# Kernel optimization log

Measured on AMD Instinct MI355X. Metric: run time of the kernel, lower is better.

## Reference

```python
import jax, jax.numpy as jnp
import numpy as np

TOP_K = 1024  # init top_k


def setup_inputs() -> dict:
    key = jax.random.key(0)
    ks = jax.random.split(key, 11)
    B, S, D, H = 8, 1024, 1024, 4096
    s = 0.02
    return {
        "inputs": jax.random.normal(ks[0], (B, S, D), jnp.float32),
        "up_w": jax.random.normal(ks[1], (H, D), jnp.float32) * s,
        "up_b": jax.random.normal(ks[2], (H,), jnp.float32) * s,
        "gate_w1": jax.random.normal(ks[3], (H, D), jnp.float32) * s,
        "gate_b1": jax.random.normal(ks[4], (H,), jnp.float32) * s,
        "gate_w2": jax.random.normal(ks[5], (H, H), jnp.float32) * s,
        "gate_b2": jax.random.normal(ks[6], (H,), jnp.float32) * s,
        "mod_w": jax.random.normal(ks[7], (H, D), jnp.float32) * s,
        "mod_b": jax.random.normal(ks[8], (H,), jnp.float32) * s,
        "down_w": jax.random.normal(ks[9], (D, H), jnp.float32) * s,
        "down_b": jax.random.normal(ks[10], (D,), jnp.float32) * s,
    }


def reference(inputs, up_w, up_b, gate_w1, gate_b1, gate_w2, gate_b2,
              mod_w, mod_b, down_w, down_b):
    B, S, D = inputs.shape
    H = up_w.shape[0]
    # gate: Linear -> ReLU -> Linear, scores [B,S,H]
    scores = jax.nn.relu(jnp.einsum('bsd,hd->bsh', inputs, gate_w1) + gate_b1)
    scores = jnp.einsum('bsh,gh->bsg', scores, gate_w2) + gate_b2
    flat_scores = scores.reshape(B, S * H)
    k = min(TOP_K * S, S * H)
    _, flat_idx = jax.lax.top_k(flat_scores, k)          # [B,k]
    hidden_idx = flat_idx % H                            # [B,k]
    # scatter writes mod.weight[h] at row h -> duplicates harmless -> boolean mask
    batch_idx = jnp.broadcast_to(jnp.arange(B)[:, None], (B, k))
    mask = jnp.zeros((B, H), bool).at[batch_idx, hidden_idx].set(True)
    # per-batch modified weights/bias (materialized like torch repeat+index_put)
    w = jnp.where(mask[:, :, None], mod_w[None], up_w[None])   # [B,H,D]
    b = jnp.where(mask, mod_b[None], up_b[None])               # [B,H]
    h = jnp.einsum('bsd,bhd->bsh', inputs, w) + b[:, None, :]
    h = jax.nn.silu(h)
    # dropout p=0.0 (eval) -> identity
    return jnp.einsum('bsh,dh->bsd', h, down_w) + down_b
```

## Files before the change

kernel.cpp:

```cpp
#include <hip/hip_runtime.h>
#include <cstdint>

typedef __attribute__((ext_vector_type(8))) short short8;
typedef __attribute__((ext_vector_type(4))) float floatx4;
typedef unsigned int uint32;

typedef const void __attribute__((address_space(1)))* gcptr;
typedef void __attribute__((address_space(3)))* lptr;

constexpr int Bn = 8, Sn = 1024, Dn = 1024, Hn = 4096;
constexpr uint32 KTOP = 1024u * 1024u;
constexpr uint32 SKBASE = 0xBB000000u;
constexpr uint32 EMAX = (1u << 27) - 1u;
constexpr uint32 WLO = 3645;
constexpr uint32 WHI = 4157;
constexpr uint32 CAP = 1u << 20;

constexpr size_t NX  = (size_t)Bn * Sn * Dn;
constexpr size_t NW1 = (size_t)Hn * Dn;
constexpr size_t NW2 = (size_t)Hn * Hn;
constexpr size_t NRS = (size_t)Bn * Sn * Hn;

constexpr size_t OFF_XH   = 0;
constexpr size_t OFF_XL   = OFF_XH  + 2 * NX;
constexpr size_t OFF_W1H  = OFF_XL  + 2 * NX;
constexpr size_t OFF_W1L  = OFF_W1H + 2 * NW1;
constexpr size_t OFF_W2H  = OFF_W1L + 2 * NW1;
constexpr size_t OFF_W2L  = OFF_W2H + 2 * NW2;
constexpr size_t OFF_RSH  = OFF_W2L + 2 * NW2;
constexpr size_t OFF_RSL  = OFF_RSH + 2 * NRS;
constexpr size_t OFF_HIST = OFF_RSL + 2 * NRS;
constexpr size_t OFF_HIST2= OFF_HIST + (size_t)Bn * 8192 * 4;
constexpr size_t OFF_HMAX = OFF_HIST2+ (size_t)Bn * 16384 * 4;
constexpr size_t OFF_META = OFF_HMAX + (size_t)Bn * Hn * 4;
constexpr size_t OFF_BSEL = OFF_META + 4096;
constexpr size_t OFF_MASK = OFF_BSEL + (size_t)Bn * Hn * 4;
constexpr size_t WS_SMALL = OFF_MASK + (size_t)Bn * Hn * 4;
constexpr size_t ZERO_BYTES = OFF_BSEL - OFF_HIST;
constexpr size_t OFF_BUF  = OFF_XL;

#define VMCNT(n) asm volatile("s_waitcnt vmcnt(" #n ")" ::: "memory")
#define SCHED0 __builtin_amdgcn_sched_barrier(0)

__device__ __forceinline__ ushort f2bf(float f) {
  uint32 u = __float_as_uint(f);
  u += 0x7fffu + ((u >> 16) & 1u);
  return (ushort)(u >> 16);
}
__device__ __forceinline__ float bf2f(ushort h) {
  return __uint_as_float(((uint32)h) << 16);
}
__device__ __forceinline__ uint32 skey(float v) {
  uint32 u = __float_as_uint(v);
  return (u & 0x80000000u) ? ~u : (u | 0x80000000u);
}
__device__ __forceinline__ uint32 ekey(uint32 key) {
  if (key <= SKBASE) return 0u;
  uint32 d = key - SKBASE;
  return d > EMAX ? EMAX : d;
}
__device__ __forceinline__ void g2l(const ushort* src, ushort* dst) {
  __builtin_amdgcn_global_load_lds((gcptr)src, (lptr)dst, 16, 0, 0);
}
__device__ __forceinline__ void stage_tile(ushort* lds, const ushort* gbase, int ldg, int tid) {
  const int w = tid >> 6;
  const int c0 = tid, c1 = tid + 256;
  g2l(gbase + (size_t)(c0 >> 2) * ldg + (c0 & 3) * 8, lds + (size_t)(w * 64) * 8);
  g2l(gbase + (size_t)(c1 >> 2) * ldg + (c1 & 3) * 8, lds + (size_t)(256 + w * 64) * 8);
}

__global__ __launch_bounds__(256) void cvt_split_k(const float4* __restrict__ x,
                                                   ushort* __restrict__ hi,
                                                   ushort* __restrict__ lo, int n4) {
  int stride = gridDim.x * 256;
  for (int i = blockIdx.x * 256 + threadIdx.x; i < n4; i += stride) {
    float4 v = x[i];
    ushort h0 = f2bf(v.x), h1 = f2bf(v.y), h2 = f2bf(v.z), h3 = f2bf(v.w);
    ushort4 hv; hv.x = h0; hv.y = h1; hv.z = h2; hv.w = h3;
    *(ushort4*)(hi + (size_t)i * 4) = hv;
    ushort4 lv;
    lv.x = f2bf(v.x - bf2f(h0)); lv.y = f2bf(v.y - bf2f(h1));
    lv.z = f2bf(v.z - bf2f(h2)); lv.w = f2bf(v.w - bf2f(h3));
    *(ushort4*)(lo + (size_t)i * 4) = lv;
  }
}
__global__ __launch_bounds__(256) void cvt_single_k(const float4* __restrict__ x,
                                                    ushort* __restrict__ hi, int n4) {
  int stride = gridDim.x * 256;
  for (int i = blockIdx.x * 256 + threadIdx.x; i < n4; i += stride) {
    float4 v = x[i];
    ushort4 hv; hv.x = f2bf(v.x); hv.y = f2bf(v.y); hv.z = f2bf(v.z); hv.w = f2bf(v.w);
    *(ushort4*)(hi + (size_t)i * 4) = hv;
  }
}
__global__ __launch_bounds__(256) void zero_out_k(float* __restrict__ o, int n) {
  int i = blockIdx.x * 256 + threadIdx.x;
  if (i < n) o[i] = 0.f;
}

constexpr int EPI_RELU = 0;
constexpr int EPI_SCORE = 1;
constexpr int EPI_SILU = 2;
constexpr int EPI_F32 = 3;

template <bool SPLIT, bool SELB, int EPI>
__global__ __launch_bounds__(256, SPLIT ? 3 : 2) void gemm_bt(
    const ushort* __restrict__ Ah, const ushort* __restrict__ Al,
    const ushort* __restrict__ Bh, const ushort* __restrict__ Bl,
    const uint32* __restrict__ bmask,
    int N, int K, long long a_bs, long long o_bs, long long bias_bs,
    const float* __restrict__ bias,
    void* __restrict__ outp, void* __restrict__ out2p) {
  __shared__ __align__(16) ushort lds[SPLIT ? 16384 : 8192];
  ushort* As = lds;
  ushort* Bs = lds + (SPLIT ? 8192 : 4096);

  const int tid = threadIdx.x;
  const int w = tid >> 6, l = tid & 63;
  const int wm = (w >> 1) << 6, wn = (w & 1) << 6;
  const int lm = l & 15, lq = l >> 4;
  const int m0 = blockIdx.y << 7, n0 = blockIdx.x << 7;
  const int z = blockIdx.z;

  const ushort* pAh = Ah + (size_t)z * a_bs + (size_t)m0 * K;
  const ushort* pBh = Bh + (size_t)n0 * K;

  floatx4 acc[4][4];
#pragma unroll
  for (int i = 0; i < 4; i++)
#pragma unroll
    for (int j = 0; j < 4; j++) acc[i][j] = floatx4{0.f, 0.f, 0.f, 0.f};

  for (int k0 = 0; k0 < K; k0 += 32) {
    stage_tile(As, pAh + k0, K, tid);
    stage_tile(Bs, pBh + k0, K, tid);
    __syncthreads();
    short8 afh[4], bfh[4];
#pragma unroll
    for (int i = 0; i < 4; i++)
      afh[i] = *(const short8*)&As[(wm + i * 16 + lm) * 32 + lq * 8];
#pragma unroll
    for (int i = 0; i < 4; i++)
      bfh[i] = *(const short8*)&Bs[(wn + i * 16 + lm) * 32 + lq * 8];
#pragma unroll
    for (int mi = 0; mi < 4; mi++)
#pragma unroll
      for (int ni = 0; ni < 4; ni++)
        acc[mi][ni] = __builtin_amdgcn_mfma_f32_16x16x32_bf16(afh[mi], bfh[ni], acc[mi][ni], 0, 0, 0);
    __syncthreads();
  }

  if constexpr (EPI == EPI_SILU) {
    ushort* o = (ushort*)outp + (size_t)z * o_bs;
    const float* bb = bias + (size_t)z * bias_bs;
#pragma unroll
    for (int mi = 0; mi < 4; mi++)
#pragma unroll
      for (int ni = 0; ni < 4; ni++) {
        int gm = m0 + wm + mi * 16 + lq * 4;
        int gn = n0 + wn + ni * 16 + lm;
        float bnv = bb[gn];
#pragma unroll
        for (int r = 0; r < 4; r++) {
          float v = acc[mi][ni][r] + bnv;
          float s = v / (1.f + __expf(-v));
          o[(size_t)(gm + r) * N + gn] = f2bf(s);
        }
      }
  } else if constexpr (EPI == EPI_F32) {
    float* o = (float*)outp;
#pragma unroll
    for (int mi = 0; mi < 4; mi++)
#pragma unroll
      for (int ni = 0; ni < 4; ni++) {
        int gm = m0 + wm + mi * 16 + lq * 4;
        int gn = n0 + wn + ni * 16 + lm;
        float bnv = bias[gn];
#pragma unroll
        for (int r = 0; r < 4; r++)
          o[(size_t)(gm + r) * N + gn] = acc[mi][ni][r] + bnv;
      }
  }
}

__device__ __forceinline__ short8 fragld(const ushort* S, int r, int swz) {
  return *(const short8*)&S[r * 32 + swz];
}
__device__ __forceinline__ void mfma_block(floatx4 (&acc)[8][4], const short8 (&af)[4],
                                           int mi0, const short8 (&bf)[4]) {
#pragma unroll
  for (int mi = 0; mi < 4; mi++)
#pragma unroll
    for (int ni = 0; ni < 4; ni++)
      acc[mi0 + mi][ni] =
          __builtin_amdgcn_mfma_f32_16x16x32_bf16(af[mi], bf[ni], acc[mi0 + mi][ni], 0, 0, 0);
}

template <bool ST>
__device__ __forceinline__ void kstep3(
    floatx4 (&acc)[8][4], ushort* ldsb, int p, int ko,
    const ushort* sAh0, const ushort* sAh1, const ushort* sBh0, const ushort* sBh1,
    const ushort* sAl0, const ushort* sAl1, const ushort* sBl0, const ushort* sBl1,
    int dbase, int swz, int lm, int wrow, int wcol,
    short8 (&ahT)[4], short8 (&bh)[4]) {
  const int q = p ^ 1;
  const ushort* AhS = ldsb + (p * 4 + 0) * 8192;
  const ushort* AlS = ldsb + (p * 4 + 2) * 8192;
  const ushort* BlS = ldsb + (p * 4 + 3) * 8192;
  ushort* dAh = ldsb + (q * 4 + 0) * 8192;
  ushort* dBh = ldsb + (q * 4 + 1) * 8192;
  ushort* dAl = ldsb + (q * 4 + 2) * 8192;
  ushort* dBl = ldsb + (q * 4 + 3) * 8192;

  short8 ahB[4], bl[4];
  __builtin_amdgcn_s_barrier();
  SCHED0;
#pragma unroll
  for (int i = 0; i < 4; i++) ahB[i] = fragld(AhS, wrow + 64 + i * 16 + lm, swz);
#pragma unroll
  for (int i = 0; i < 4; i++) bl[i] = fragld(BlS, wcol + i * 16 + lm, swz);
  if constexpr (ST) {
    g2l(sAh0 + ko, dAh + dbase); g2l(sAh1 + ko, dAh + dbase + 4096);
    g2l(sBh0 + ko, dBh + dbase); g2l(sBh1 + ko, dBh + dbase + 4096);
    g2l(sBl0 + ko, dBl + dbase); g2l(sBl1 + ko, dBl + dbase + 4096);
  }
  SCHED0;
  __builtin_amdgcn_s_setprio(1);
  mfma_block(acc, ahT, 0, bh);
  mfma_block(acc, ahB, 4, bh);
  __builtin_amdgcn_s_setprio(0);
  if constexpr (ST) VMCNT(6); else VMCNT(0);

  short8 alT[4], alB[4];
  __builtin_amdgcn_s_barrier();
  SCHED0;
#pragma unroll
  for (int i = 0; i < 4; i++) alT[i] = fragld(AlS, wrow + i * 16 + lm, swz);
#pragma unroll
  for (int i = 0; i < 4; i++) alB[i] = fragld(AlS, wrow + 64 + i * 16 + lm, swz);
  if constexpr (ST) {
    g2l(sAl0 + ko, dAl + dbase); g2l(sAl1 + ko, dAl + dbase + 4096);
  }
  SCHED0;
  __builtin_amdgcn_s_setprio(1);
  mfma_block(acc, ahT, 0, bl);
  mfma_block(acc, ahB, 4, bl);
  __builtin_amdgcn_s_setprio(0);
  if constexpr (ST) VMCNT(4);

  __builtin_amdgcn_s_barrier();
  SCHED0;
  short8 ahTn[4], bhn[4];
  if constexpr (ST) {
    const ushort* AhSn = ldsb + (q * 4 + 0) * 8192;
    const ushort* BhSn = ldsb + (q * 4 + 1) * 8192;
#pragma unroll
    for (int i = 0; i < 4; i++) ahTn[i] = fragld(AhSn, wrow + i * 16 + lm, swz);
#pragma unroll
    for (int i = 0; i < 4; i++) bhn[i] = fragld(BhSn, wcol + i * 16 + lm, swz);
  }
  SCHED0;
  __builtin_amdgcn_s_setprio(1);
  mfma_block(acc, alT, 0, bh);
  mfma_block(acc, alB, 4, bh);
  __builtin_amdgcn_s_setprio(0);
  if constexpr (ST) {
    VMCNT(2);
#pragma unroll
    for (int i = 0; i < 4; i++) { ahT[i] = ahTn[i]; bh[i] = bhn[i]; }
  }
}

template <bool ST>
__device__ __forceinline__ void kstep_ns(
    floatx4 (&acc)[8][4], ushort* ldsb, int p, int ko,
    const ushort* sA0, const ushort* sA1, const ushort* sB0, const ushort* sB1,
    int dbase, int swz, int lm, int wrow, int wcol) {
  const ushort* AS = ldsb + (p * 2 + 0) * 8192;
  const ushort* BS = ldsb + (p * 2 + 1) * 8192;
  ushort* dA = ldsb + ((p ^ 1) * 2 + 0) * 8192;
  ushort* dB = ldsb + ((p ^ 1) * 2 + 1) * 8192;
  short8 aT[4], aB[4], b[4];
#pragma unroll
  for (int i = 0; i < 4; i++) aT[i] = fragld(AS, wrow + i * 16 + lm, swz);
#pragma unroll
  for (int i = 0; i < 4; i++) b[i]  = fragld(BS, wcol + i * 16 + lm, swz);
#pragma unroll
  for (int i = 0; i < 4; i++) aB[i] = fragld(AS, wrow + 64 + i * 16 + lm, swz);
  if constexpr (ST) {
    g2l(sA0 + ko, dA + dbase); g2l(sA1 + ko, dA + dbase + 4096);
    g2l(sB0 + ko, dB + dbase); g2l(sB1 + ko, dB + dbase + 4096);
  }
  __builtin_amdgcn_s_barrier();
  __builtin_amdgcn_s_setprio(1);
  mfma_block(acc, aT, 0, b);
  __builtin_amdgcn_s_setprio(0);
  __builtin_amdgcn_s_barrier();
  __builtin_amdgcn_s_setprio(1);
  mfma_block(acc, aB, 4, b);
  __builtin_amdgcn_s_setprio(0);
  if constexpr (ST) VMCNT(0);
  __builtin_amdgcn_s_barrier();
}

template <int EPI, bool SPLIT, bool SELB>
__global__ __launch_bounds__(512, 2) void gemm256(
    const ushort* __restrict__ Ah, const ushort* __restrict__ Al,
    const ushort* __restrict__ Bh, const ushort* __restrict__ Bl,
    const uint32* __restrict__ bmask,
    int N, int K, long long a_bs, long long o_bs, long long bias_bs,
    const float* __restrict__ bias,
    ushort* __restrict__ outh, ushort* __restrict__ outl,
    uint32* __restrict__ hist, uint32* __restrict__ hmax,
    uint32* __restrict__ buf, uint32* __restrict__ cnt) {
  static_assert(EPI != EPI_SCORE || SPLIT, "score path is split");
  static_assert(!(SPLIT && SELB), "unused combo");
  constexpr int NSUB = SPLIT ? 4 : 2;
  __shared__ __align__(16) ushort lds[2 * NSUB * 8192];
  ushort* ldsb = &lds[0];

  const int tid = threadIdx.x;
  const int l = tid & 63, w = tid >> 6;
  const int lm = l & 15, lq = l >> 4;
  const int swz = (lq ^ ((lm >> 1) & 3)) << 3;
  const int wrow = (w >> 2) << 7, wcol = (w & 3) << 6;
  const int m0 = blockIdx.y << 8, n0 = blockIdx.x << 8;
  const int z = blockIdx.z;

  const int cg = ((l & 3) ^ ((l >> 3) & 3)) << 3;
  const int r0 = (w << 4) + (l >> 2);
  const size_t soff0 = (size_t)r0 * K + cg;
  const size_t soff1 = soff0 + (size_t)128 * K;
  const int dbase = w << 9;

  const ushort* pA = Ah + (size_t)z * a_bs + (size_t)m0 * K;
  const ushort* sAh0 = pA + soff0;
  const ushort* sAh1 = pA + soff1;
  const ushort* sAl0 = nullptr;
  const ushort* sAl1 = nullptr;
  if constexpr (SPLIT) {
    const ushort* pAl = Al + (size_t)z * a_bs + (size_t)m0 * K;
    sAl0 = pAl + soff0;
    sAl1 = pAl + soff1;
  }
  const ushort* sBh0;
  const ushort* sBh1;
  if constexpr (SELB) {
    const uint32* bm = bmask + (size_t)z * Hn;
    const int gr0 = n0 + r0, gr1 = gr0 + 128;
    sBh0 = (bm[gr0] ? Bl : Bh) + (size_t)gr0 * K + cg;
    sBh1 = (bm[gr1] ? Bl : Bh) + (size_t)gr1 * K + cg;
  } else {
    sBh0 = Bh + (size_t)n0 * K + soff0;
    sBh1 = Bh + (size_t)n0 * K + soff1;
  }
  const ushort* sBl0 = nullptr;
  const ushort* sBl1 = nullptr;
  if constexpr (SPLIT) {
    sBl0 = Bl + (size_t)n0 * K + soff0;
    sBl1 = Bl + (size_t)n0 * K + soff1;
  }

  floatx4 acc[8][4];
#pragma unroll
  for (int i = 0; i < 8; i++)
#pragma unroll
    for (int j = 0; j < 4; j++) acc[i][j] = floatx4{0.f, 0.f, 0.f, 0.f};

  const int nk = K >> 5;

  if constexpr (SPLIT) {
    g2l(sAh0, ldsb + 0 * 8192 + dbase); g2l(sAh1, ldsb + 0 * 8192 + dbase + 4096);
    g2l(sBh0, ldsb + 1 * 8192 + dbase); g2l(sBh1, ldsb + 1 * 8192 + dbase + 4096);
    g2l(sBl0, ldsb + 3 * 8192 + dbase); g2l(sBl1, ldsb + 3 * 8192 + dbase + 4096);
    g2l(sAl0, ldsb + 2 * 8192 + dbase); g2l(sAl1, ldsb + 2 * 8192 + dbase + 4096);
    VMCNT(2);
    __builtin_amdgcn_s_barrier();
    SCHED0;
    short8 ahT[4], bh[4];
#pragma unroll
    for (int i = 0; i < 4; i++) ahT[i] = fragld(ldsb + 0 * 8192, wrow + i * 16 + lm, swz);
#pragma unroll
    for (int i = 0; i < 4; i++) bh[i]  = fragld(ldsb + 1 * 8192, wcol + i * 16 + lm, swz);
    int T = 0;
    for (; T < nk - 1; ++T)
      kstep3<true>(acc, ldsb, T & 1, (T + 1) << 5, sAh0, sAh1, sBh0, sBh1,
                   sAl0, sAl1, sBl0, sBl1, dbase, swz, lm, wrow, wcol, ahT, bh);
    kstep3<false>(acc, ldsb, T & 1, 0, sAh0, sAh1, sBh0, sBh1,
                  sAl0, sAl1, sBl0, sBl1, dbase, swz, lm, wrow, wcol, ahT, bh);
  } else {
    g2l(sAh0, ldsb + 0 * 8192 + dbase); g2l(sAh1, ldsb + 0 * 8192 + dbase + 4096);
    g2l(sBh0, ldsb + 1 * 8192 + dbase); g2l(sBh1, ldsb + 1 * 8192 + dbase + 4096);
    VMCNT(0);
    __builtin_amdgcn_s_barrier();
    int T = 0;
    for (; T < nk - 1; ++T)
      kstep_ns<true>(acc, ldsb, T & 1, (T + 1) << 5, sAh0, sAh1, sBh0, sBh1,
                     dbase, swz, lm, wrow, wcol);
    kstep_ns<false>(acc, ldsb, T & 1, 0, sAh0, sAh1, sBh0, sBh1,
                    dbase, swz, lm, wrow, wcol);
  }

  if constexpr (EPI == EPI_RELU) {
#pragma unroll
    for (int mi = 0; mi < 8; mi++)
#pragma unroll
      for (int ni = 0; ni < 4; ni++) {
        const int gm = m0 + wrow + mi * 16 + lq * 4;
        const int gn = n0 + wcol + ni * 16 + lm;
        const float bnv = bias[gn];
#pragma unroll
        for (int r = 0; r < 4; r++) {
          float v = fmaxf(acc[mi][ni][r] + bnv, 0.f);
          ushort h = f2bf(v);
          size_t o = (size_t)(gm + r) * N + gn;
          outh[o] = h;
          outl[o] = f2bf(v - bf2f(h));
        }
      }
  } else if constexpr (EPI == EPI_SILU) {
    ushort* o = outh + (size_t)z * o_bs;
    const float* bb = bias + (size_t)z * bias_bs;
#pragma unroll
    for (int mi = 0; mi < 8; mi++)
#pragma unroll
      for (int ni = 0; ni < 4; ni++) {
        const int gm = m0 + wrow + mi * 16 + lq * 4;
        const int gn = n0 + wcol + ni * 16 + lm;
        const float bnv = bb[gn];
#pragma unroll
        for (int r = 0; r < 4; r++) {
          float v = acc[mi][ni][r] + bnv;
          float s = v / (1.f + __expf(-v));
          o[(size_t)(gm + r) * N + gn] = f2bf(s);
        }
      }
  } else if constexpr (EPI == EPI_SCORE) {
    __syncthreads();
    uint32* hs = (uint32*)ldsb;
    for (int i = tid; i < 8192; i += 512) hs[i] = 0;
    __syncthreads();
    const int batch = m0 >> 10;
    uint32 cntl = 0;
#pragma unroll
    for (int ni = 0; ni < 4; ni++) {
      const int gn = n0 + wcol + ni * 16 + lm;
      const float bnv = bias[gn];
      float vmax = -3.4e38f;
#pragma unroll
      for (int mi = 0; mi < 8; mi++) {
#pragma unroll
        for (int r = 0; r < 4; r++) {
          float v = acc[mi][ni][r] + bnv;
          uint32 e = ekey(skey(v));
          uint32 bk = e >> 14;
          atomicAdd(&hs[bk], 1u);
          if (bk >= WLO && bk <= WHI) cntl++;
          vmax = fmaxf(vmax, v);
        }
      }
      atomicMax(&hmax[batch * Hn + gn], skey(vmax));
    }
    __syncthreads();
    for (int i = tid; i < 8192; i += 512) {
      uint32 c = hs[i];
      if (c) atomicAdd(&hist[batch * 8192 + i], c);
    }
    __syncthreads();
    hs[tid] = cntl;
    __syncthreads();
    if (tid == 0) {
      uint32 run = 0;
      for (int i = 0; i < 512; i++) { uint32 t = hs[i]; hs[i] = run; run += t; }
      hs[512] = atomicAdd(&cnt[batch], run);
    }
    __syncthreads();
    uint32 off = hs[512] + hs[tid];
    uint32* bb = buf + (size_t)batch * CAP;
#pragma unroll
    for (int ni = 0; ni < 4; ni++) {
      const int gn = n0 + wcol + ni * 16 + lm;
      const float bnv = bias[gn];
#pragma unroll
      for (int mi = 0; mi < 8; mi++) {
#pragma unroll
        for (int r = 0; r < 4; r++) {
          float v = acc[mi][ni][r] + bnv;
          uint32 e = ekey(skey(v));
          uint32 bk = e >> 14;
          if (bk >= WLO && bk <= WHI) {
            if (off < CAP) bb[off] = e;
            off++;
          }
        }
      }
    }
  }
}

__global__ __launch_bounds__(256) void select1_k(const uint32* __restrict__ hist,
                                                 uint32* __restrict__ meta) {
  int b = blockIdx.x;
  const uint32* h = hist + b * 8192;
  __shared__ uint32 ps[256];
  uint32 s = 0;
  int base = threadIdx.x * 32;
  for (int i = 0; i < 32; i++) s += h[base + i];
  ps[threadIdx.x] = s;
  __syncthreads();
  if (threadIdx.x == 0) {
    uint32 cum = 0, need = 1;
    int j = 0;
    for (int c = 255; c >= 0; c--) {
      if (cum + ps[c] >= KTOP) {
        for (int i = c * 32 + 31;; i--) {
          uint32 hv = h[i];
          if (cum + hv >= KTOP) { j = i; need = KTOP - cum; break; }
          cum += hv;
        }
        break;
      }
      cum += ps[c];
    }
    meta[8 + b] = (uint32)j;
    meta[16 + b] = need;
    meta[b] = SKBASE + ((uint32)j << 14);
  }
}

__global__ __launch_bounds__(256) void refine_buf_k(const uint32* __restrict__ buf,
                                                    const uint32* __restrict__ meta,
                                                    uint32* __restrict__ hist2) {
  const uint32* cnt = meta + 32;
  size_t stride = (size_t)gridDim.x * 256;
  for (int b = 0; b < Bn; b++) {
    uint32 n = cnt[b] < CAP ? cnt[b] : CAP;
    uint32 j = meta[8 + b];
    const uint32* bb = buf + (size_t)b * CAP;
    for (size_t i = (size_t)blockIdx.x * 256 + threadIdx.x; i < n; i += stride) {
      uint32 e = bb[i];
      if ((e >> 14) == j) atomicAdd(&hist2[(size_t)b * 16384 + (e & 0x3FFFu)], 1u);
    }
  }
}

__global__ __launch_bounds__(256) void select2_k(const uint32* __restrict__ hist2,
                                                 uint32* __restrict__ meta) {
  int b = blockIdx.x;
  const uint32* h2 = hist2 + (size_t)b * 16384;
  __shared__ uint32 ps[256];
  uint32 s = 0;
  const uint32* p = h2 + (size_t)threadIdx.x * 64;
  for (int i = 0; i < 64; i += 4) {
    uint4 v = *(const uint4*)(p + i);
    s += v.x + v.y + v.z + v.w;
  }
  ps[threadIdx.x] = s;
  __syncthreads();
  if (threadIdx.x == 0) {
    uint32 j = meta[8 + b];
    uint32 valid = (j >= WLO && j <= WHI && meta[32 + b] <= CAP) ? 1u : 0u;
    if (valid) {
      uint32 need = meta[16 + b];
      uint32 cum = 0;
      int c = 255;
      for (; c > 0; c--) {
        if (cum + ps[c] >= need) break;
        cum += ps[c];
      }
      uint32 rem = 0;
      for (int i = 63; i >= 0; i--) {
        uint32 hv = h2[c * 64 + i];
        if (cum + hv >= need) { rem = (uint32)(c * 64 + i); break; }
        cum += hv;
      }
      meta[b] = SKBASE + (j << 14) + rem;
    }
  }
}

__global__ __launch_bounds__(256) void mask_k(const uint32* __restrict__ hmax,
                                              const uint32* __restrict__ meta,
                                              const float* __restrict__ modb,
                                              const float* __restrict__ upb,
                                              uint32* __restrict__ mask,
                                              float* __restrict__ bsel) {
  int i = blockIdx.x * 256 + threadIdx.x;
  int b = i >> 12, h = i & 4095;
  bool m = hmax[i] >= meta[b];
  mask[i] = m ? 1u : 0u;
  bsel[i] = m ? modb[h] : upb[h];
}

extern "C" void kernel_launch(void* const* d_in, const int* in_sizes, int n_in,
                              void* d_out, int out_size, void* d_ws, size_t ws_size,
                              hipStream_t stream) {
  (void)in_sizes; (void)n_in;
  const float* x    = (const float*)d_in[0];
  const float* up_w = (const float*)d_in[1];
  const float* up_b = (const float*)d_in[2];
  const float* g_w1 = (const float*)d_in[3];
  const float* g_b1 = (const float*)d_in[4];
  const float* g_w2 = (const float*)d_in[5];
  const float* g_b2 = (const float*)d_in[6];
  const float* mod_w= (const float*)d_in[7];
  const float* mod_b= (const float*)d_in[8];
  const float* dw   = (const float*)d_in[9];
  const float* db   = (const float*)d_in[10];
  float* out = (float*)d_out;

  if (ws_size < WS_SMALL) {
    zero_out_k<<<(out_size + 255) / 256, 256, 0, stream>>>(out, out_size);
    return;
  }

  char* ws = (char*)d_ws;
  ushort* XH  = (ushort*)(ws + OFF_XH);
  ushort* XL  = (ushort*)(ws + OFF_XL);
  ushort* W1H = (ushort*)(ws + OFF_W1H);
  ushort* W1L = (ushort*)(ws + OFF_W1L);
  ushort* W2H = (ushort*)(ws + OFF_W2H);
  ushort* W2L = (ushort*)(ws + OFF_W2L);
  ushort* RSH = (ushort*)(ws + OFF_RSH);
  ushort* RSL = (ushort*)(ws + OFF_RSL);
  uint32* HIST = (uint32*)(ws + OFF_HIST);
  uint32* HIST2= (uint32*)(ws + OFF_HIST2);
  uint32* HMAX = (uint32*)(ws + OFF_HMAX);
  uint32* META = (uint32*)(ws + OFF_META);
  float*  BSEL = (float*)(ws + OFF_BSEL);
  uint32* MASK = (uint32*)(ws + OFF_MASK);
  uint32* BUF  = (uint32*)(ws + OFF_BUF);
  ushort* UPW  = W1H;
  ushort* MODW = W1L;
  ushort* DWNW = XL;
  ushort* HBUF = RSH;

  hipMemsetAsync(ws + OFF_HIST, 0, ZERO_BYTES, stream);

  cvt_split_k<<<1024, 256, 0, stream>>>((const float4*)x, XH, XL, (int)(NX / 4));
  cvt_split_k<<<1024, 256, 0, stream>>>((const float4*)g_w1, W1H, W1L, (int)(NW1 / 4));
  cvt_split_k<<<2048, 256, 0, stream>>>((const float4*)g_w2, W2H, W2L, (int)(NW2 / 4));

  gemm256<EPI_RELU, true, false><<<dim3(Hn / 256, (Bn * Sn) / 256), 512, 0, stream>>>(
      XH, XL, W1H, W1L, nullptr, Hn, Dn, 0, 0, 0, g_b1, RSH, RSL,
      nullptr, nullptr, nullptr, nullptr);
  gemm256<EPI_SCORE, true, false><<<dim3(Hn / 256, (Bn * Sn) / 256), 512, 0, stream>>>(
      RSH, RSL, W2H, W2L, nullptr, Hn, Hn, 0, 0, 0, g_b2, nullptr, nullptr,
      HIST, HMAX, BUF, META + 32);

  select1_k<<<Bn, 256, 0, stream>>>(HIST, META);
  refine_buf_k<<<512, 256, 0, stream>>>(BUF, META, HIST2);
  select2_k<<<Bn, 256, 0, stream>>>(HIST2, META);
  mask_k<<<(Bn * Hn) / 256, 256, 0, stream>>>(HMAX, META, mod_b, up_b, MASK, BSEL);

  cvt_single_k<<<1024, 256, 0, stream>>>((const float4*)up_w, UPW, (int)(NW1 / 4));
  cvt_single_k<<<1024, 256, 0, stream>>>((const float4*)mod_w, MODW, (int)(NW1 / 4));
  cvt_single_k<<<1024, 256, 0, stream>>>((const float4*)dw, DWNW, (int)(NW1 / 4));

  gemm256<EPI_SILU, false, true><<<dim3(Hn / 256, Sn / 256, Bn), 512, 0, stream>>>(
      XH, nullptr, UPW, MODW, MASK, Hn, Dn,
      (long long)Sn * Dn, (long long)Sn * Hn, (long long)Hn,
      BSEL, HBUF, nullptr, nullptr, nullptr, nullptr, nullptr);
  gemm_bt<false, false, EPI_F32><<<dim3(Dn / 128, (Bn * Sn) / 128, 1), 256, 0, stream>>>(
      HBUF, nullptr, DWNW, nullptr, nullptr, Dn, Hn, 0, 0, 0, db, out, nullptr);
}
```

Measured before the change: 1.272 ms.

## Load split-precision A fragments directly from global into registers, skip LDS staging

```diff
diff --git a/kernel.cpp b/kernel.cpp
--- a/kernel.cpp
+++ b/kernel.cpp
@@ -197,78 +197,53 @@
 }
 
 template <bool ST>
-__device__ __forceinline__ void kstep3(
-    floatx4 (&acc)[8][4], ushort* ldsb, int p, int ko,
-    const ushort* sAh0, const ushort* sAh1, const ushort* sBh0, const ushort* sBh1,
-    const ushort* sAl0, const ushort* sAl1, const ushort* sBl0, const ushort* sBl1,
-    int dbase, int swz, int lm, int wrow, int wcol,
-    short8 (&ahT)[4], short8 (&bh)[4]) {
-  const int q = p ^ 1;
-  const ushort* AhS = ldsb + (p * 4 + 0) * 8192;
-  const ushort* AlS = ldsb + (p * 4 + 2) * 8192;
-  const ushort* BlS = ldsb + (p * 4 + 3) * 8192;
-  ushort* dAh = ldsb + (q * 4 + 0) * 8192;
-  ushort* dBh = ldsb + (q * 4 + 1) * 8192;
-  ushort* dAl = ldsb + (q * 4 + 2) * 8192;
-  ushort* dBl = ldsb + (q * 4 + 3) * 8192;
-
-  short8 ahB[4], bl[4];
+__device__ __forceinline__ void kstep_sp2(
+    floatx4 (&acc)[8][4], ushort* ldsb, int p, long long k0, long long kn,
+    const ushort* __restrict__ aH, const ushort* __restrict__ aL, long long Kll,
+    const ushort* sBh0, const ushort* sBh1, const ushort* sBl0, const ushort* sBl1,
+    int dbase, int swz, int lm, int wcol, short8 (&ah)[8]) {
+  const ushort* BhS = ldsb + (p * 2 + 0) * 8192;
+  const ushort* BlS = ldsb + (p * 2 + 1) * 8192;
+  ushort* dBh = ldsb + ((p ^ 1) * 2 + 0) * 8192;
+  ushort* dBl = ldsb + ((p ^ 1) * 2 + 1) * 8192;
+
   __builtin_amdgcn_s_barrier();
   SCHED0;
-#pragma unroll
-  for (int i = 0; i < 4; i++) ahB[i] = fragld(AhS, wrow + 64 + i * 16 + lm, swz);
+  short8 al[8];
+#pragma unroll
+  for (int i = 0; i < 8; i++)
+    al[i] = *(const short8*)(aL + (long long)(i * 16) * Kll + k0);
+  short8 bh[4], bl[4];
+#pragma unroll
+  for (int i = 0; i < 4; i++) bh[i] = fragld(BhS, wcol + i * 16 + lm, swz);
 #pragma unroll
   for (int i = 0; i < 4; i++) bl[i] = fragld(BlS, wcol + i * 16 + lm, swz);
   if constexpr (ST) {
-    g2l(sAh0 + ko, dAh + dbase); g2l(sAh1 + ko, dAh + dbase + 4096);
-    g2l(sBh0 + ko, dBh + dbase); g2l(sBh1 + ko, dBh + dbase + 4096);
-    g2l(sBl0 + ko, dBl + dbase); g2l(sBl1 + ko, dBl + dbase + 4096);
+    g2l(sBh0 + kn, dBh + dbase); g2l(sBh1 + kn, dBh + dbase + 4096);
+    g2l(sBl0 + kn, dBl + dbase); g2l(sBl1 + kn, dBl + dbase + 4096);
   }
   SCHED0;
   __builtin_amdgcn_s_setprio(1);
-  mfma_block(acc, ahT, 0, bh);
-  mfma_block(acc, ahB, 4, bh);
+  mfma_block(acc, *(const short8(*)[4])&ah[0], 0, bh);
+  mfma_block(acc, *(const short8(*)[4])&ah[4], 4, bh);
   __builtin_amdgcn_s_setprio(0);
-  if constexpr (ST) VMCNT(6); else VMCNT(0);
-
-  short8 alT[4], alB[4];
-  __builtin_amdgcn_s_barrier();
-  SCHED0;
-#pragma unroll
-  for (int i = 0; i < 4; i++) alT[i] = fragld(AlS, wrow + i * 16 + lm, swz);
-#pragma unroll
-  for (int i = 0; i < 4; i++) alB[i] = fragld(AlS, wrow + 64 + i * 16 + lm, swz);
-  if constexpr (ST) {
-    g2l(sAl0 + ko, dAl + dbase); g2l(sAl1 + ko, dAl + dbase + 4096);
-  }
   SCHED0;
   __builtin_amdgcn_s_setprio(1);
-  mfma_block(acc, ahT, 0, bl);
-  mfma_block(acc, ahB, 4, bl);
+  mfma_block(acc, *(const short8(*)[4])&ah[0], 0, bl);
+  mfma_block(acc, *(const short8(*)[4])&ah[4], 4, bl);
   __builtin_amdgcn_s_setprio(0);
-  if constexpr (ST) VMCNT(4);
-
-  __builtin_amdgcn_s_barrier();
   SCHED0;
-  short8 ahTn[4], bhn[4];
   if constexpr (ST) {
-    const ushort* AhSn = ldsb + (q * 4 + 0) * 8192;
-    const ushort* BhSn = ldsb + (q * 4 + 1) * 8192;
-#pragma unroll
-    for (int i = 0; i < 4; i++) ahTn[i] = fragld(AhSn, wrow + i * 16 + lm, swz);
-#pragma unroll
-    for (int i = 0; i < 4; i++) bhn[i] = fragld(BhSn, wcol + i * 16 + lm, swz);
+#pragma unroll
+    for (int i = 0; i < 8; i++)
+      ah[i] = *(const short8*)(aH + (long long)(i * 16) * Kll + kn);
   }
   SCHED0;
   __builtin_amdgcn_s_setprio(1);
-  mfma_block(acc, alT, 0, bh);
-  mfma_block(acc, alB, 4, bh);
+  mfma_block(acc, *(const short8(*)[4])&al[0], 0, bh);
+  mfma_block(acc, *(const short8(*)[4])&al[4], 4, bh);
   __builtin_amdgcn_s_setprio(0);
-  if constexpr (ST) {
-    VMCNT(2);
-#pragma unroll
-    for (int i = 0; i < 4; i++) { ahT[i] = ahTn[i]; bh[i] = bhn[i]; }
-  }
+  if constexpr (ST) VMCNT(8);
 }
 
 template <bool ST>
@@ -315,8 +290,7 @@
     uint32* __restrict__ buf, uint32* __restrict__ cnt) {
   static_assert(EPI != EPI_SCORE || SPLIT, "score path is split");
   static_assert(!(SPLIT && SELB), "unused combo");
-  constexpr int NSUB = SPLIT ? 4 : 2;
-  __shared__ __align__(16) ushort lds[2 * NSUB * 8192];
+  __shared__ __align__(16) ushort lds[2 * 2 * 8192];
   ushort* ldsb = &lds[0];
 
   const int tid = threadIdx.x;
@@ -333,16 +307,6 @@
   const size_t soff1 = soff0 + (size_t)128 * K;
   const int dbase = w << 9;
 
-  const ushort* pA = Ah + (size_t)z * a_bs + (size_t)m0 * K;
-  const ushort* sAh0 = pA + soff0;
-  const ushort* sAh1 = pA + soff1;
-  const ushort* sAl0 = nullptr;
-  const ushort* sAl1 = nullptr;
-  if constexpr (SPLIT) {
-    const ushort* pAl = Al + (size_t)z * a_bs + (size_t)m0 * K;
-    sAl0 = pAl + soff0;
-    sAl1 = pAl + soff1;
-  }
   const ushort* sBh0;
   const ushort* sBh1;
   if constexpr (SELB) {
@@ -370,25 +334,28 @@
   const int nk = K >> 5;
 
   if constexpr (SPLIT) {
-    g2l(sAh0, ldsb + 0 * 8192 + dbase); g2l(sAh1, ldsb + 0 * 8192 + dbase + 4096);
-    g2l(sBh0, ldsb + 1 * 8192 + dbase); g2l(sBh1, ldsb + 1 * 8192 + dbase + 4096);
-    g2l(sBl0, ldsb + 3 * 8192 + dbase); g2l(sBl1, ldsb + 3 * 8192 + dbase + 4096);
-    g2l(sAl0, ldsb + 2 * 8192 + dbase); g2l(sAl1, ldsb + 2 * 8192 + dbase + 4096);
-    VMCNT(2);
-    __builtin_amdgcn_s_barrier();
-    SCHED0;
-    short8 ahT[4], bh[4];
-#pragma unroll
-    for (int i = 0; i < 4; i++) ahT[i] = fragld(ldsb + 0 * 8192, wrow + i * 16 + lm, swz);
-#pragma unroll
-    for (int i = 0; i < 4; i++) bh[i]  = fragld(ldsb + 1 * 8192, wcol + i * 16 + lm, swz);
+    const ushort* aH = Ah + (size_t)z * a_bs + (size_t)(m0 + wrow + lm) * K + lq * 8;
+    const ushort* aL = Al + (size_t)z * a_bs + (size_t)(m0 + wrow + lm) * K + lq * 8;
+    const long long Kll = K;
+
+    g2l(sBh0, ldsb + 0 * 8192 + dbase); g2l(sBh1, ldsb + 0 * 8192 + dbase + 4096);
+    g2l(sBl0, ldsb + 1 * 8192 + dbase); g2l(sBl1, ldsb + 1 * 8192 + dbase + 4096);
+    short8 ah[8];
+#pragma unroll
+    for (int i = 0; i < 8; i++)
+      ah[i] = *(const short8*)(aH + (long long)(i * 16) * Kll);
+    VMCNT(0);
+
     int T = 0;
     for (; T < nk - 1; ++T)
-      kstep3<true>(acc, ldsb, T & 1, (T + 1) << 5, sAh0, sAh1, sBh0, sBh1,
-                   sAl0, sAl1, sBl0, sBl1, dbase, swz, lm, wrow, wcol, ahT, bh);
-    kstep3<false>(acc, ldsb, T & 1, 0, sAh0, sAh1, sBh0, sBh1,
-                  sAl0, sAl1, sBl0, sBl1, dbase, swz, lm, wrow, wcol, ahT, bh);
+      kstep_sp2<true>(acc, ldsb, T & 1, (long long)T << 5, (long long)(T + 1) << 5,
+                      aH, aL, Kll, sBh0, sBh1, sBl0, sBl1, dbase, swz, lm, wcol, ah);
+    kstep_sp2<false>(acc, ldsb, T & 1, (long long)T << 5, 0,
+                     aH, aL, Kll, sBh0, sBh1, sBl0, sBl1, dbase, swz, lm, wcol, ah);
   } else {
+    const ushort* pA = Ah + (size_t)z * a_bs + (size_t)m0 * K;
+    const ushort* sAh0 = pA + soff0;
+    const ushort* sAh1 = pA + soff1;
     g2l(sAh0, ldsb + 0 * 8192 + dbase); g2l(sAh1, ldsb + 0 * 8192 + dbase + 4096);
     g2l(sBh0, ldsb + 1 * 8192 + dbase); g2l(sBh1, ldsb + 1 * 8192 + dbase + 4096);
     VMCNT(0);
```

New measurement: 1.819 ms. 1.43x slower.
